# Kernel tuning notes

Measured on AMD Instinct MI355X. Metric: run time of the kernel, lower is better.

Reference implementation:

```python
import jax, jax.numpy as jnp
import numpy as np

N_NODES = 100000
N_EDGES = 1000000
IN_FEATS = 256
OUT_FEATS = 64


def setup_inputs() -> dict:
    key = jax.random.key(0)
    k1, k2, k3, k4 = jax.random.split(key, 4)
    x = jax.random.normal(k1, (N_NODES, IN_FEATS), dtype=jnp.float32)
    src = jax.random.randint(k2, (N_EDGES,), 0, N_NODES, dtype=jnp.int64)
    dst = jax.random.randint(k3, (N_EDGES,), 0, N_NODES, dtype=jnp.int64)
    # Glorot-style init as in dgl GraphConv
    W = jax.random.normal(k4, (IN_FEATS, OUT_FEATS), dtype=jnp.float32) * (2.0 / (IN_FEATS + OUT_FEATS)) ** 0.5
    b = jnp.zeros((OUT_FEATS,), dtype=jnp.float32)
    return {"x": x, "src": src, "dst": dst, "W": W, "b": b}


def reference(x, src, dst, W, b):
    # dgl GraphConv with norm='both':
    #   h = D_in^{-1/2} * A * D_out^{-1/2} * X * W + b
    # in_feats > out_feats -> dense transform first, then sparse aggregation.
    n = x.shape[0]
    e_ones = jnp.ones(src.shape[0], dtype=x.dtype)
    deg_out = jnp.clip(jax.ops.segment_sum(e_ones, src, num_segments=n), 1.0)  # [N]
    deg_in = jnp.clip(jax.ops.segment_sum(e_ones, dst, num_segments=n), 1.0)   # [N]
    h = (x * deg_out[:, None] ** -0.5) @ W                 # [N, out]
    agg = jax.ops.segment_sum(h[src], dst, num_segments=n)  # SpMM: [N, out]
    return agg * deg_in[:, None] ** -0.5 + b
```

## Files before the change

kernel.cpp:

```cpp
#include <hip/hip_runtime.h>

#define IN_F 256
#define OUT_F 64
#define BLK1 128
#define BKT 128
#define CAP 4096

typedef __attribute__((ext_vector_type(8))) short s16x8;
typedef __attribute__((ext_vector_type(4))) float f32x4;
typedef __attribute__((ext_vector_type(4))) unsigned u32x4;

__device__ __forceinline__ unsigned short bf16_rne(float f) {
    unsigned u = __builtin_bit_cast(unsigned, f);
    u += 0x7FFFu + ((u >> 16) & 1u);
    return (unsigned short)(u >> 16);
}
__device__ __forceinline__ float bf16_lo(unsigned u) {
    return __builtin_bit_cast(float, u << 16);
}
__device__ __forceinline__ float bf16_hi(unsigned u) {
    return __builtin_bit_cast(float, u & 0xFFFF0000u);
}
__device__ __forceinline__ unsigned pk2(float a, float b) {
    unsigned r;
    asm("v_cvt_pk_bf16_f32 %0, %1, %2" : "=v"(r) : "v"(a), "v"(b));
    return r;
}

__global__ __launch_bounds__(1024) void k_coarse(const int* __restrict__ src,
                                                 const int* __restrict__ dst,
                                                 int* __restrict__ cnt,
                                                 int nb, int ne) {
    __shared__ int hD[1024], hS[1024];
    const int blk = blockIdx.x, tid = threadIdx.x;
    hD[tid] = 0; hS[tid] = 0;
    __syncthreads();
    const int epb = (ne + BLK1 - 1) / BLK1;
    const int e0 = blk * epb, e1 = min(ne, e0 + epb);
    for (int e = e0 + tid; e < e1; e += 1024) {
        atomicAdd(&hD[dst[e] >> 7], 1);
        atomicAdd(&hS[src[e] >> 7], 1);
    }
    __syncthreads();
    for (int bb = tid; bb < nb; bb += 1024) {
        cnt[bb * BLK1 + blk] = hD[bb];
        cnt[(nb + bb) * BLK1 + blk] = hS[bb];
    }
}

__global__ __launch_bounds__(256) void k_scan1(const int* __restrict__ deg,
                                               int* __restrict__ excl,
                                               int* __restrict__ partials, int m) {
    __shared__ int sd[256];
    const int tid = threadIdx.x;
    const int idx = blockIdx.x * 1024 + tid * 4;
    int v0 = 0, v1 = 0, v2 = 0, v3 = 0;
    if (idx     < m) v0 = deg[idx];
    if (idx + 1 < m) v1 = deg[idx + 1];
    if (idx + 2 < m) v2 = deg[idx + 2];
    if (idx + 3 < m) v3 = deg[idx + 3];
    const int tsum = v0 + v1 + v2 + v3;
    sd[tid] = tsum;
    __syncthreads();
    for (int off = 1; off < 256; off <<= 1) {
        int t = (tid >= off) ? sd[tid - off] : 0;
        __syncthreads();
        sd[tid] += t;
        __syncthreads();
    }
    int run = sd[tid] - tsum;
    if (tid == 255) partials[blockIdx.x] = sd[255];
    if (idx     < m) { excl[idx]     = run; run += v0; }
    if (idx + 1 < m) { excl[idx + 1] = run; run += v1; }
    if (idx + 2 < m) { excl[idx + 2] = run; run += v2; }
    if (idx + 3 < m) { excl[idx + 3] = run; }
}

__global__ __launch_bounds__(256) void k_scan2(int* __restrict__ partials, int nb) {
    __shared__ int sd[256];
    const int tid = threadIdx.x;
    const int v = (tid < nb) ? partials[tid] : 0;
    sd[tid] = v;
    __syncthreads();
    for (int off = 1; off < 256; off <<= 1) {
        int t = (tid >= off) ? sd[tid - off] : 0;
        __syncthreads();
        sd[tid] += t;
        __syncthreads();
    }
    if (tid < nb) partials[tid] = sd[tid] - v;
}

__global__ __launch_bounds__(1024) void k_part(const int* __restrict__ src,
                                               const int* __restrict__ dst,
                                               const int* __restrict__ cnt,
                                               const int* __restrict__ partials,
                                               unsigned* __restrict__ tmpD,
                                               unsigned char* __restrict__ tmpS,
                                               int nb, int ne) {
    __shared__ int cD[1024], cS[1024];
    const int blk = blockIdx.x, tid = threadIdx.x;
    for (int bb = tid; bb < nb; bb += 1024) {
        int iD = bb * BLK1 + blk;
        int iS = (nb + bb) * BLK1 + blk;
        cD[bb] = cnt[iD] + partials[iD >> 10];
        cS[bb] = cnt[iS] + partials[iS >> 10];
    }
    __syncthreads();
    const int epb = (ne + BLK1 - 1) / BLK1;
    const int e0 = blk * epb, e1 = min(ne, e0 + epb);
    for (int e = e0 + tid; e < e1; e += 1024) {
        int d = dst[e], s = src[e];
        int pD = atomicAdd(&cD[d >> 7], 1);
        tmpD[pD] = ((unsigned)(d & 127) << 17) | (unsigned)s;
        int pS = atomicAdd(&cS[s >> 7], 1);
        tmpS[pS - ne] = (unsigned char)(s & 127);
    }
}

__global__ __launch_bounds__(256, 4) void k_gemm(const float* __restrict__ x,
                                                 const float* __restrict__ W,
                                                 const int* __restrict__ cnt,
                                                 const int* __restrict__ partials,
                                                 const unsigned char* __restrict__ tmpS,
                                                 unsigned short* __restrict__ h,
                                                 int n, int nb, int ne) {
    __shared__ char lds[32768];
    __shared__ int hist[BKT];
    const int tid = threadIdx.x;
    const int lane = tid & 63;
    const int wid = tid >> 6;
    const int b = blockIdx.x;

    if (tid < BKT) hist[tid] = 0;
    __syncthreads();
    {
        const int ib = (nb + b) * BLK1;
        const int base = cnt[ib] + partials[ib >> 10] - ne;
        const int ie2 = (nb + b + 1) * BLK1;
        const int end = (b + 1 < nb) ? (cnt[ie2] + partials[ie2 >> 10] - ne) : ne;
        for (int i = base + tid; i < end; i += 256)
            atomicAdd(&hist[tmpS[i] & 127u], 1);
    }
    {
        const int f = tid & 63;
        const int kg = (tid >> 6) * 64;
        const int swz = (f & 7) << 4;
#pragma unroll
        for (int j = 0; j < 16; ++j) {
            const int k0 = kg + j * 4;
            float w0 = W[(k0 + 0) * OUT_F + f];
            float w1 = W[(k0 + 1) * OUT_F + f];
            float w2 = W[(k0 + 2) * OUT_F + f];
            float w3 = W[(k0 + 3) * OUT_F + f];
            uint2 p;
            p.x = pk2(w0, w1);
            p.y = pk2(w2, w3);
            *(uint2*)(lds + f * 512 + ((k0 * 2) ^ swz)) = p;
        }
    }
    __syncthreads();

    const int r15 = lane & 15;
    const int q = lane >> 4;
    const int bswz = (r15 & 7) << 4;
    const int b_base = r15 * 512;
    const int rq = q * 4;

#pragma unroll
    for (int p = 0; p < 2; ++p) {
        const int row = b * 128 + p * 64 + wid * 16 + r15;
        const int rowc = min(row, n - 1);
        const float* xr = x + (size_t)rowc * IN_F + q * 8;

        f32x4 acc0 = {0.f, 0.f, 0.f, 0.f};
        f32x4 acc1 = acc0, acc2 = acc0, acc3 = acc0;

#pragma unroll
        for (int kk = 0; kk < 8; ++kk) {
            float4 a0 = *(const float4*)(xr + kk * 32);
            float4 a1 = *(const float4*)(xr + kk * 32 + 4);
            u32x4 au;
            au[0] = pk2(a0.x, a0.y);
            au[1] = pk2(a0.z, a0.w);
            au[2] = pk2(a1.x, a1.y);
            au[3] = pk2(a1.z, a1.w);
            s16x8 a = __builtin_bit_cast(s16x8, au);
            const int off = (q * 16 + kk * 64) ^ bswz;
            s16x8 b0 = *(const s16x8*)(lds + b_base + off);
            s16x8 b1 = *(const s16x8*)(lds + b_base + 8192 + off);
            s16x8 b2 = *(const s16x8*)(lds + b_base + 16384 + off);
            s16x8 b3 = *(const s16x8*)(lds + b_base + 24576 + off);
            acc0 = __builtin_amdgcn_mfma_f32_16x16x32_bf16(a, b0, acc0, 0, 0, 0);
            acc1 = __builtin_amdgcn_mfma_f32_16x16x32_bf16(a, b1, acc1, 0, 0, 0);
            acc2 = __builtin_amdgcn_mfma_f32_16x16x32_bf16(a, b2, acc2, 0, 0, 0);
            acc3 = __builtin_amdgcn_mfma_f32_16x16x32_bf16(a, b3, acc3, 0, 0, 0);
        }

#pragma unroll
        for (int j = 0; j < 4; ++j) {
            const int grow = b * 128 + p * 64 + wid * 16 + rq + j;
            if (grow < n) {
                const float s = rsqrtf(fmaxf((float)hist[grow & 127], 1.0f));
                unsigned short* hp = h + (size_t)grow * OUT_F + r15;
                hp[0]  = bf16_rne(acc0[j] * s);
                hp[16] = bf16_rne(acc1[j] * s);
                hp[32] = bf16_rne(acc2[j] * s);
                hp[48] = bf16_rne(acc3[j] * s);
            }
        }
    }
}

__global__ __launch_bounds__(512) void k_agg(const int* __restrict__ cnt,
                                             const int* __restrict__ partials,
                                             const unsigned* __restrict__ tmpD,
                                             const unsigned* __restrict__ h32,
                                             const float* __restrict__ b,
                                             float* __restrict__ out,
                                             int n, int nb, int ne) {
    __shared__ int hist[BKT], sd[BKT], cur[BKT], stt[BKT];
    __shared__ unsigned raw[CAP];
    __shared__ int eidx[CAP];
    const int bkt = blockIdx.x, tid = threadIdx.x;
    const int ib = bkt * BLK1;
    const int base = cnt[ib] + partials[ib >> 10];
    const int ie = (bkt + 1) * BLK1;
    const int end = (bkt + 1 < nb) ? (cnt[ie] + partials[ie >> 10]) : ne;
    const int cnt_e = min(end - base, CAP);

    if (tid < BKT) hist[tid] = 0;
    __syncthreads();
    for (int i = tid; i < cnt_e; i += 512) {
        unsigned v = tmpD[base + i];
        raw[i] = v;
        atomicAdd(&hist[v >> 17], 1);
    }
    __syncthreads();
    int dg0 = 0;
    if (tid < BKT) { dg0 = hist[tid]; sd[tid] = dg0; }
    __syncthreads();
    for (int off = 1; off < BKT; off <<= 1) {
        int t = 0;
        if (tid < BKT && tid >= off) t = sd[tid - off];
        __syncthreads();
        if (tid < BKT) sd[tid] += t;
        __syncthreads();
    }
    if (tid < BKT) {
        const int excl = sd[tid] - dg0;
        cur[tid] = excl;
        stt[tid] = excl;
    }
    __syncthreads();
    for (int i = tid; i < cnt_e; i += 512) {
        unsigned v = raw[i];
        int pos = atomicAdd(&cur[v >> 17], 1);
        eidx[min(pos, CAP - 1)] = (int)(v & 0x1FFFFu);
    }
    __syncthreads();

    const int wid = tid >> 6, lane = tid & 63;
    const int f2 = lane & 31, half = lane >> 5;
    for (int nd = wid; nd < BKT; nd += 8) {
        const int node = bkt * BKT + nd;
        if (node >= n) continue;
        const int st = stt[nd];
        const int dg = hist[nd];
        float a0 = 0.f, a1 = 0.f, c0 = 0.f, c1 = 0.f;
        float d0 = 0.f, d1 = 0.f, e0 = 0.f, e1 = 0.f;
        int i = 0;
        const int dg8 = dg & ~7;
        for (; i < dg8; i += 8) {
            int s0 = eidx[st + i + half];
            int s1 = eidx[st + i + 2 + half];
            int s2 = eidx[st + i + 4 + half];
            int s3 = eidx[st + i + 6 + half];
            unsigned u0 = h32[s0 * 32 + f2];
            unsigned u1 = h32[s1 * 32 + f2];
            unsigned u2 = h32[s2 * 32 + f2];
            unsigned u3 = h32[s3 * 32 + f2];
            a0 += bf16_lo(u0); a1 += bf16_hi(u0);
            c0 += bf16_lo(u1); c1 += bf16_hi(u1);
            d0 += bf16_lo(u2); d1 += bf16_hi(u2);
            e0 += bf16_lo(u3); e1 += bf16_hi(u3);
        }
        for (; i < dg; i += 2) {
            const int e = i + half;
            const bool v = e < dg;
            int s = eidx[st + (v ? e : i)];
            unsigned u = h32[s * 32 + f2];
            if (v) { a0 += bf16_lo(u); a1 += bf16_hi(u); }
        }
        a0 += c0; a1 += c1;
        d0 += e0; d1 += e1;
        a0 += d0; a1 += d1;
        a0 += __shfl_xor(a0, 32, 64);
        a1 += __shfl_xor(a1, 32, 64);
        if (half == 0) {
            const float scale = rsqrtf(fmaxf((float)dg, 1.0f));
            float2 v;
            v.x = a0 * scale + b[f2 * 2];
            v.y = a1 * scale + b[f2 * 2 + 1];
            *(float2*)&out[(size_t)node * OUT_F + f2 * 2] = v;
        }
    }
}

extern "C" void kernel_launch(void* const* d_in, const int* in_sizes, int n_in,
                              void* d_out, int out_size, void* d_ws, size_t ws_size,
                              hipStream_t stream) {
    const float* x   = (const float*)d_in[0];
    const int*   src = (const int*)d_in[1];
    const int*   dst = (const int*)d_in[2];
    const float* W   = (const float*)d_in[3];
    const float* b   = (const float*)d_in[4];
    float* out = (float*)d_out;

    const int n  = in_sizes[0] / IN_F;
    const int ne = in_sizes[1];

    const int nb = (n + BKT - 1) / BKT;
    const int m  = 2 * nb * BLK1;

    int* cnt          = (int*)d_ws;
    int* partials     = cnt + m;
    unsigned* tmpD    = (unsigned*)(partials + 256);
    unsigned char* tmpS = (unsigned char*)(tmpD + ne);
    unsigned short* h = (unsigned short*)(tmpS + (((size_t)ne + 15) & ~(size_t)15));

    const int nb_scan = (m + 1023) / 1024;

    k_coarse<<<BLK1, 1024, 0, stream>>>(src, dst, cnt, nb, ne);
    k_scan1<<<nb_scan, 256, 0, stream>>>(cnt, cnt, partials, m);
    k_scan2<<<1, 256, 0, stream>>>(partials, nb_scan);
    k_part<<<BLK1, 1024, 0, stream>>>(src, dst, cnt, partials, tmpD, tmpS, nb, ne);
    k_gemm<<<nb, 256, 0, stream>>>(x, W, cnt, partials, tmpS, h, n, nb, ne);
    k_agg<<<nb, 512, 0, stream>>>(cnt, partials, tmpD, (const unsigned*)h, b, out, n, nb, ne);
}
```

Before: 101.7 us.

## Fuse scan passes with last-block pattern and slim aggregation blocks to 256 threads

```diff
diff --git a/kernel.cpp b/kernel.cpp
--- a/kernel.cpp
+++ b/kernel.cpp
@@ -30,9 +30,11 @@
 __global__ __launch_bounds__(1024) void k_coarse(const int* __restrict__ src,
                                                  const int* __restrict__ dst,
                                                  int* __restrict__ cnt,
+                                                 int* __restrict__ counter,
                                                  int nb, int ne) {
     __shared__ int hD[1024], hS[1024];
     const int blk = blockIdx.x, tid = threadIdx.x;
+    if (blk == 0 && tid == 0) *counter = 0;
     hD[tid] = 0; hS[tid] = 0;
     __syncthreads();
     const int epb = (ne + BLK1 - 1) / BLK1;
@@ -50,8 +52,11 @@
 
 __global__ __launch_bounds__(256) void k_scan1(const int* __restrict__ deg,
                                                int* __restrict__ excl,
-                                               int* __restrict__ partials, int m) {
+                                               int* __restrict__ partials,
+                                               int* __restrict__ counter,
+                                               int m, int nsc) {
     __shared__ int sd[256];
+    __shared__ int lastf;
     const int tid = threadIdx.x;
     const int idx = blockIdx.x * 1024 + tid * 4;
     int v0 = 0, v1 = 0, v2 = 0, v3 = 0;
@@ -74,21 +79,28 @@
     if (idx + 1 < m) { excl[idx + 1] = run; run += v1; }
     if (idx + 2 < m) { excl[idx + 2] = run; run += v2; }
     if (idx + 3 < m) { excl[idx + 3] = run; }
-}
-
-__global__ __launch_bounds__(256) void k_scan2(int* __restrict__ partials, int nb) {
-    __shared__ int sd[256];
-    const int tid = threadIdx.x;
-    const int v = (tid < nb) ? partials[tid] : 0;
-    sd[tid] = v;
-    __syncthreads();
-    for (int off = 1; off < 256; off <<= 1) {
-        int t = (tid >= off) ? sd[tid - off] : 0;
-        __syncthreads();
-        sd[tid] += t;
-        __syncthreads();
-    }
-    if (tid < nb) partials[tid] = sd[tid] - v;
+
+    __threadfence();
+    if (tid == 0) {
+        int d = atomicAdd(counter, 1);
+        lastf = (d == (int)gridDim.x - 1) ? 1 : 0;
+    }
+    __syncthreads();
+    if (lastf) {
+        int v = 0;
+        if (tid < nsc)
+            v = __hip_atomic_load(&partials[tid], __ATOMIC_RELAXED,
+                                  __HIP_MEMORY_SCOPE_AGENT);
+        sd[tid] = v;
+        __syncthreads();
+        for (int off = 1; off < 256; off <<= 1) {
+            int t = (tid >= off) ? sd[tid - off] : 0;
+            __syncthreads();
+            sd[tid] += t;
+            __syncthreads();
+        }
+        if (tid < nsc) partials[tid] = sd[tid] - v;
+    }
 }
 
 __global__ __launch_bounds__(1024) void k_part(const int* __restrict__ src,
@@ -212,15 +224,14 @@
     }
 }
 
-__global__ __launch_bounds__(512) void k_agg(const int* __restrict__ cnt,
-                                             const int* __restrict__ partials,
-                                             const unsigned* __restrict__ tmpD,
-                                             const unsigned* __restrict__ h32,
-                                             const float* __restrict__ b,
-                                             float* __restrict__ out,
-                                             int n, int nb, int ne) {
+__global__ __launch_bounds__(256, 8) void k_agg(const int* __restrict__ cnt,
+                                                const int* __restrict__ partials,
+                                                const unsigned* __restrict__ tmpD,
+                                                const unsigned* __restrict__ h32,
+                                                const float* __restrict__ b,
+                                                float* __restrict__ out,
+                                                int n, int nb, int ne) {
     __shared__ int hist[BKT], sd[BKT], cur[BKT], stt[BKT];
-    __shared__ unsigned raw[CAP];
     __shared__ int eidx[CAP];
     const int bkt = blockIdx.x, tid = threadIdx.x;
     const int ib = bkt * BLK1;
@@ -231,11 +242,8 @@
 
     if (tid < BKT) hist[tid] = 0;
     __syncthreads();
-    for (int i = tid; i < cnt_e; i += 512) {
-        unsigned v = tmpD[base + i];
-        raw[i] = v;
-        atomicAdd(&hist[v >> 17], 1);
-    }
+    for (int i = tid; i < cnt_e; i += 256)
+        atomicAdd(&hist[tmpD[base + i] >> 17], 1);
     __syncthreads();
     int dg0 = 0;
     if (tid < BKT) { dg0 = hist[tid]; sd[tid] = dg0; }
@@ -253,8 +261,8 @@
         stt[tid] = excl;
     }
     __syncthreads();
-    for (int i = tid; i < cnt_e; i += 512) {
-        unsigned v = raw[i];
+    for (int i = tid; i < cnt_e; i += 256) {
+        unsigned v = tmpD[base + i];
         int pos = atomicAdd(&cur[v >> 17], 1);
         eidx[min(pos, CAP - 1)] = (int)(v & 0x1FFFFu);
     }
@@ -262,7 +270,7 @@
 
     const int wid = tid >> 6, lane = tid & 63;
     const int f2 = lane & 31, half = lane >> 5;
-    for (int nd = wid; nd < BKT; nd += 8) {
+    for (int nd = wid; nd < BKT; nd += 4) {
         const int node = bkt * BKT + nd;
         if (node >= n) continue;
         const int st = stt[nd];
@@ -325,16 +333,16 @@
 
     int* cnt          = (int*)d_ws;
     int* partials     = cnt + m;
-    unsigned* tmpD    = (unsigned*)(partials + 256);
+    int* counter      = partials + 256;
+    unsigned* tmpD    = (unsigned*)(counter + 15);
     unsigned char* tmpS = (unsigned char*)(tmpD + ne);
     unsigned short* h = (unsigned short*)(tmpS + (((size_t)ne + 15) & ~(size_t)15));
 
     const int nb_scan = (m + 1023) / 1024;
 
-    k_coarse<<<BLK1, 1024, 0, stream>>>(src, dst, cnt, nb, ne);
-    k_scan1<<<nb_scan, 256, 0, stream>>>(cnt, cnt, partials, m);
-    k_scan2<<<1, 256, 0, stream>>>(partials, nb_scan);
+    k_coarse<<<BLK1, 1024, 0, stream>>>(src, dst, cnt, counter, nb, ne);
+    k_scan1<<<nb_scan, 256, 0, stream>>>(cnt, cnt, partials, counter, m, nb_scan);
     k_part<<<BLK1, 1024, 0, stream>>>(src, dst, cnt, partials, tmpD, tmpS, nb, ne);
     k_gemm<<<nb, 256, 0, stream>>>(x, W, cnt, partials, tmpS, h, n, nb, ne);
-    k_agg<<<nb, 512, 0, stream>>>(cnt, partials, tmpD, (const unsigned*)h, b, out, n, nb, ne);
-}
+    k_agg<<<nb, 256, 0, stream>>>(cnt, partials, tmpD, (const unsigned*)h, b, out, n, nb, ne);
+}
```

Result: slower. 143.2 us (+40.9%).
